# Kernel tuning notes

Measured on AMD Instinct MI355X. Metric: run time of the kernel, lower is better.

Reference implementation:

```python
import jax, jax.numpy as jnp
import numpy as np

N_NODES = 100000
N_EDGES = 1600000
F_IN, HIDDEN, N_CLASS = 256, 64, 2


def _gcn_conv(x, W, b, src, dst, norm, n):
    # PyG GCNConv: linear (no bias) -> normalized scatter-add -> bias
    h = x @ W                                  # [N, out]
    msg = h[src] * norm[:, None]               # gather + scale, [E+N, out]
    agg = jax.ops.segment_sum(msg, dst, num_segments=n)
    return agg + b


def setup_inputs() -> dict:
    key = jax.random.key(0)
    ks = jax.random.split(key, 8)
    x = jax.random.normal(ks[0], (N_NODES, F_IN), dtype=jnp.float32)
    edge_index = jax.random.randint(ks[1], (2, N_EDGES), 0, N_NODES, dtype=jnp.int32)
    W1 = jax.random.normal(ks[2], (F_IN, HIDDEN), dtype=jnp.float32) / np.sqrt(F_IN).astype(np.float32)
    b1 = jnp.zeros((HIDDEN,), dtype=jnp.float32)
    W2 = jax.random.normal(ks[3], (HIDDEN, HIDDEN), dtype=jnp.float32) / np.sqrt(HIDDEN).astype(np.float32)
    b2 = jnp.zeros((HIDDEN,), dtype=jnp.float32)
    W3 = jax.random.normal(ks[4], (HIDDEN, N_CLASS), dtype=jnp.float32) / np.sqrt(HIDDEN).astype(np.float32)
    b3 = jnp.zeros((N_CLASS,), dtype=jnp.float32)
    return {"x": x, "edge_index": edge_index, "W1": W1, "b1": b1, "W2": W2, "b2": b2, "W3": W3, "b3": b3}


def reference(x, edge_index, W1, b1, W2, b2, W3, b3):
    n = x.shape[0]
    # add self-loops (GCNConv default)
    loops = jnp.arange(n, dtype=edge_index.dtype)
    src = jnp.concatenate([edge_index[0], loops])
    dst = jnp.concatenate([edge_index[1], loops])
    # symmetric normalization D^-1/2 A_hat D^-1/2
    deg = jax.ops.segment_sum(jnp.ones_like(src, dtype=x.dtype), dst, num_segments=n)
    deg_inv_sqrt = jnp.where(deg > 0, jax.lax.rsqrt(jnp.maximum(deg, 1.0)), 0.0)
    norm = deg_inv_sqrt[src] * deg_inv_sqrt[dst]
    # layer 1 + relu (dropout is identity in eval mode)
    h = jax.nn.relu(_gcn_conv(x, W1, b1, src, dst, norm, n))
    # layer 2 + relu
    h = jax.nn.relu(_gcn_conv(h, W2, b2, src, dst, norm, n))
    # output layer + log_softmax
    h = _gcn_conv(h, W3, b3, src, dst, norm, n)
    return jax.nn.log_softmax(h, axis=1)
```

## Files before the change

kernel.cpp:

```cpp
#include <hip/hip_runtime.h>
#include <math.h>

#define F_IN 256
#define HID  64
#define BSH  8
#define BSPAN 256
#define CHUNK 4096
#define NBK_MAX 512

typedef __bf16   bf16x8 __attribute__((ext_vector_type(8)));
typedef float    floatx4 __attribute__((ext_vector_type(4)));
typedef _Float16 half8 __attribute__((ext_vector_type(8)));
typedef _Float16 half4v __attribute__((ext_vector_type(4)));

__global__ __launch_bounds__(256) void k_hist(const int* __restrict__ dst,
                                              int* __restrict__ cntT,
                                              int E, int NCH, int NBK) {
    __shared__ int hist[NBK_MAX];
    int t = threadIdx.x, c = blockIdx.x;
    hist[t] = 0; hist[t + 256] = 0;
    __syncthreads();
    int base = c * CHUNK;
#pragma unroll 4
    for (int j = 0; j < CHUNK / 256; j++) {
        int e = base + j * 256 + t;
        if (e < E) atomicAdd(&hist[dst[e] >> BSH], 1);
    }
    __syncthreads();
    for (int b = t; b < NBK; b += 256) cntT[b * NCH + c] = hist[b];
}

__global__ __launch_bounds__(256) void k_scanA(const int* __restrict__ cntT,
                                               int* __restrict__ off,
                                               int* __restrict__ partials, int S) {
    __shared__ int sh[256];
    int tid = threadIdx.x;
    int base = blockIdx.x * 1024 + tid * 4;
    int v[4];
    int s = 0;
#pragma unroll
    for (int j = 0; j < 4; j++) {
        int idx = base + j;
        v[j] = (idx < S) ? cntT[idx] : 0;
        s += v[j];
    }
    sh[tid] = s;
    __syncthreads();
    int mysum = s;
    for (int o = 1; o < 256; o <<= 1) {
        int tv = (tid >= o) ? sh[tid - o] : 0;
        __syncthreads();
        sh[tid] += tv;
        __syncthreads();
    }
    int pref = sh[tid] - mysum;
#pragma unroll
    for (int j = 0; j < 4; j++) {
        int idx = base + j;
        if (idx < S) off[idx] = pref;
        pref += v[j];
    }
    if (tid == 255) partials[blockIdx.x] = sh[255];
}

__global__ void k_scanB(int* __restrict__ partials, int* __restrict__ off,
                        int nblk, int S) {
    if (blockIdx.x == 0 && threadIdx.x == 0) {
        int run = 0;
        for (int b = 0; b < nblk; b++) { int t = partials[b]; partials[b] = run; run += t; }
        off[S] = run;
    }
}

__global__ void k_scanC(int* __restrict__ off, const int* __restrict__ partials, int S) {
    int i = blockIdx.x * blockDim.x + threadIdx.x;
    if (i < S) off[i] += partials[i >> 10];
}

__global__ __launch_bounds__(256) void k_sortwrite(const int* __restrict__ src,
                                                   const int* __restrict__ dst,
                                                   const int* __restrict__ off,
                                                   int* __restrict__ ebuf,
                                                   int E, int NCH, int NBK) {
    __shared__ int cur[NBK_MAX];
    int t = threadIdx.x, c = blockIdx.x;
    for (int b = t; b < NBK; b += 256) cur[b] = off[b * NCH + c];
    __syncthreads();
    int base = c * CHUNK;
#pragma unroll 4
    for (int j = 0; j < CHUNK / 256; j++) {
        int e = base + j * 256 + t;
        if (e < E) {
            int s = src[e];
            int d = dst[e];
            int pos = atomicAdd(&cur[d >> BSH], 1);
            ebuf[pos] = (s << BSH) | (d & (BSPAN - 1));
        }
    }
}

__global__ __launch_bounds__(256) void k_bucket_csr(const int* __restrict__ off,
                                                    const int* __restrict__ ebuf,
                                                    int* __restrict__ rp,
                                                    float* __restrict__ dinv,
                                                    int* __restrict__ esrc,
                                                    int N, int NCH, int NBK) {
    __shared__ int cnt[BSPAN];
    __shared__ int sh[BSPAN];
    int b = blockIdx.x, t = threadIdx.x;
    int base = off[b * NCH];
    int end  = off[(b + 1) * NCH];

    cnt[t] = 0;
    __syncthreads();
    for (int i = base + t; i < end; i += 256) atomicAdd(&cnt[ebuf[i] & (BSPAN - 1)], 1);
    __syncthreads();

    int c = cnt[t];
    sh[t] = c;
    __syncthreads();
    for (int o = 1; o < 256; o <<= 1) {
        int tv = (t >= o) ? sh[t - o] : 0;
        __syncthreads();
        sh[t] += tv;
        __syncthreads();
    }
    int excl = sh[t] - c;

    int node = (b << BSH) + t;
    if (node < N) {
        rp[node] = base + excl;
        dinv[node] = rsqrtf((float)(1 + c));
    }
    if (b == NBK - 1 && t == 0) rp[N] = end;
    __syncthreads();

    cnt[t] = base + excl;
    __syncthreads();
    for (int i = base + t; i < end; i += 256) {
        int v = ebuf[i];
        int p = atomicAdd(&cnt[v & (BSPAN - 1)], 1);
        esrc[p] = v >> BSH;
    }
}

__global__ __launch_bounds__(256) void k_prepw(const float* __restrict__ W1,
                                               __bf16* __restrict__ f1h, __bf16* __restrict__ f1l,
                                               const float* __restrict__ W2,
                                               __bf16* __restrict__ f2h, __bf16* __restrict__ f2l) {
    int t = threadIdx.x + blockIdx.x * blockDim.x;
    for (int idx = t; idx < 16384; idx += 2048) {
        int j = idx & 7, lane = (idx >> 3) & 63, ch2 = (idx >> 9) & 7, c = idx >> 12;
        int k = ch2 * 32 + (lane >> 4) * 8 + j, col = c * 16 + (lane & 15);
        float w = W1[k * 64 + col];
        __bf16 h = (__bf16)w;
        f1h[idx] = h; f1l[idx] = (__bf16)(w - (float)h);
    }
    for (int idx = t; idx < 4096; idx += 2048) {
        int j = idx & 7, lane = (idx >> 3) & 63, ch2 = (idx >> 9) & 1, c = idx >> 10;
        int k = ch2 * 32 + (lane >> 4) * 8 + j, col = c * 16 + (lane & 15);
        float w = W2[k * 64 + col];
        __bf16 h = (__bf16)w;
        f2h[idx] = h; f2l[idx] = (__bf16)(w - (float)h);
    }
}

__global__ __launch_bounds__(256) void k_gemm1(const float* __restrict__ A,
                                               const __bf16* __restrict__ BfH,
                                               const __bf16* __restrict__ BfL,
                                               const float* __restrict__ dinv,
                                               _Float16* __restrict__ C, int nrows) {
    constexpr int K = 256, KC = 64, NCHK = 4, NCH32 = 8;
    __shared__ float As[2][64 * KC];

    const int t = threadIdx.x;
    const int wave = t >> 6, lane = t & 63;
    const int m = lane & 15, q = lane >> 4;
    const int row0 = blockIdx.x * 64;

    const int s_sub = lane >> 4;
    const int s_seg = lane & 15;

    auto stage = [&](int ch, int buf) {
#pragma unroll
        for (int j = 0; j < 4; j++) {
            int lr = wave * 16 + j * 4 + s_sub;
            int gr = row0 + lr; if (gr > nrows - 1) gr = nrows - 1;
            int gs = (s_seg - lr) & 15;
            const float* g = A + (size_t)gr * K + ch * KC + gs * 4;
            float* l = &As[buf][(size_t)lr * KC + s_seg * 4];
            __builtin_amdgcn_global_load_lds(
                (const __attribute__((address_space(1))) void*)g,
                (__attribute__((address_space(3))) void*)l, 16, 0, 0);
        }
    };

    floatx4 acc[4] = {{0.f, 0.f, 0.f, 0.f}, {0.f, 0.f, 0.f, 0.f},
                      {0.f, 0.f, 0.f, 0.f}, {0.f, 0.f, 0.f, 0.f}};

    stage(0, 0);
    __syncthreads();

    for (int ch = 0; ch < NCHK; ch++) {
        if (ch + 1 < NCHK) stage(ch + 1, (ch + 1) & 1);

        const float* arow = &As[ch & 1][(size_t)(wave * 16 + m) * KC];
#pragma unroll
        for (int jj = 0; jj < 2; jj++) {
            int ch2 = ch * 2 + jj;
            int s0 = jj * 8 + q * 2;
            float4 v0 = *(const float4*)(arow + (((s0 + m) & 15) * 4));
            float4 v1 = *(const float4*)(arow + (((s0 + 1 + m) & 15) * 4));
            float af[8] = {v0.x, v0.y, v0.z, v0.w, v1.x, v1.y, v1.z, v1.w};
            bf16x8 ah, al;
#pragma unroll
            for (int j = 0; j < 8; j++) {
                __bf16 h = (__bf16)af[j];
                ah[j] = h;
                al[j] = (__bf16)(af[j] - (float)h);
            }
#pragma unroll
            for (int c = 0; c < 4; c++) {
                const bf16x8 bh = *(const bf16x8*)(BfH + ((size_t)(c * NCH32 + ch2) * 64 + lane) * 8);
                const bf16x8 bl = *(const bf16x8*)(BfL + ((size_t)(c * NCH32 + ch2) * 64 + lane) * 8);
                acc[c] = __builtin_amdgcn_mfma_f32_16x16x32_bf16(ah, bh, acc[c], 0, 0, 0);
                acc[c] = __builtin_amdgcn_mfma_f32_16x16x32_bf16(al, bh, acc[c], 0, 0, 0);
                acc[c] = __builtin_amdgcn_mfma_f32_16x16x32_bf16(ah, bl, acc[c], 0, 0, 0);
            }
        }
        __syncthreads();
    }

#pragma unroll
    for (int i = 0; i < 4; i++) {
        int r = row0 + wave * 16 + q * 4 + i;
        if (r < nrows) {
            float di = dinv[r];
#pragma unroll
            for (int c = 0; c < 4; c++)
                C[(size_t)r * 64 + c * 16 + m] = (_Float16)(acc[c][i] * di);
        }
    }
}

__global__ __launch_bounds__(256) void k_gemm2(const _Float16* __restrict__ A,
                                               const __bf16* __restrict__ BfH,
                                               const __bf16* __restrict__ BfL,
                                               const float* __restrict__ dinv,
                                               _Float16* __restrict__ C, int nrows) {
    __shared__ _Float16 As[64 * 64];
    const int t = threadIdx.x;
    const int wave = t >> 6, lane = t & 63;
    const int m = lane & 15, q = lane >> 4;
    const int row0 = blockIdx.x * 64;

#pragma unroll
    for (int j = 0; j < 2; j++) {
        int lr = j * 32 + wave * 8 + (lane >> 3);
        int p  = lane & 7;
        int gr = row0 + lr; if (gr > nrows - 1) gr = nrows - 1;
        int gs = (p - lr) & 7;
        const _Float16* g = A + (size_t)gr * 64 + gs * 8;
        _Float16* l = &As[(size_t)lr * 64 + p * 8];
        __builtin_amdgcn_global_load_lds(
            (const __attribute__((address_space(1))) void*)g,
            (__attribute__((address_space(3))) void*)l, 16, 0, 0);
    }
    __syncthreads();

    floatx4 acc[4] = {{0.f, 0.f, 0.f, 0.f}, {0.f, 0.f, 0.f, 0.f},
                      {0.f, 0.f, 0.f, 0.f}, {0.f, 0.f, 0.f, 0.f}};

    const _Float16* arow = &As[(size_t)(wave * 16 + m) * 64];
#pragma unroll
    for (int jj = 0; jj < 2; jj++) {
        int s0 = jj * 4 + q;
        half8 v = *(const half8*)(arow + (((s0 + m) & 7) * 8));
        bf16x8 ah, al;
#pragma unroll
        for (int j = 0; j < 8; j++) {
            float f = (float)v[j];
            __bf16 h = (__bf16)f;
            ah[j] = h;
            al[j] = (__bf16)(f - (float)h);
        }
#pragma unroll
        for (int c = 0; c < 4; c++) {
            const bf16x8 bh = *(const bf16x8*)(BfH + ((size_t)(c * 2 + jj) * 64 + lane) * 8);
            const bf16x8 bl = *(const bf16x8*)(BfL + ((size_t)(c * 2 + jj) * 64 + lane) * 8);
            acc[c] = __builtin_amdgcn_mfma_f32_16x16x32_bf16(ah, bh, acc[c], 0, 0, 0);
            acc[c] = __builtin_amdgcn_mfma_f32_16x16x32_bf16(al, bh, acc[c], 0, 0, 0);
            acc[c] = __builtin_amdgcn_mfma_f32_16x16x32_bf16(ah, bl, acc[c], 0, 0, 0);
        }
    }

#pragma unroll
    for (int i = 0; i < 4; i++) {
        int r = row0 + wave * 16 + q * 4 + i;
        if (r < nrows) {
            float di = dinv[r];
#pragma unroll
            for (int c = 0; c < 4; c++)
                C[(size_t)r * 64 + c * 16 + m] = (_Float16)(acc[c][i] * di);
        }
    }
}

template <int MODE>
__global__ __launch_bounds__(256) void k_agg64(const _Float16* __restrict__ hs,
                                               const float* __restrict__ dinv,
                                               const int* __restrict__ rp,
                                               const int* __restrict__ esrc,
                                               const float* __restrict__ bias,
                                               const float* __restrict__ W3,
                                               void* __restrict__ out, int n) {
    int lane = threadIdx.x & 63;
    int qe = lane >> 4;
    int fg = lane & 15;
    int nid = blockIdx.x * 4 + (threadIdx.x >> 6);
    if (nid >= n) return;
    nid = __builtin_amdgcn_readfirstlane(nid);

    float dii = dinv[nid];
    int e0 = rp[nid];
    int e1 = rp[nid + 1];
    int last = e1 - 1;

    float a0 = 0.f, a1 = 0.f, a2 = 0.f, a3 = 0.f;
    if (qe == 0) {
        half4v sv = *(const half4v*)(hs + (size_t)nid * 64 + fg * 4);
        a0 = (float)sv[0]; a1 = (float)sv[1]; a2 = (float)sv[2]; a3 = (float)sv[3];
    }

    for (int e = e0; e <= last; e += 16) {
#pragma unroll
        for (int u = 0; u < 4; u++) {
            int slot = e + u * 4 + qe;
            int idx = esrc[min(slot, last)];
            half4v v = *(const half4v*)(hs + (size_t)idx * 64 + fg * 4);
            if (slot <= last) {
                a0 += (float)v[0]; a1 += (float)v[1];
                a2 += (float)v[2]; a3 += (float)v[3];
            }
        }
    }

#pragma unroll
    for (int o = 16; o <= 32; o <<= 1) {
        a0 += __shfl_xor(a0, o, 64);
        a1 += __shfl_xor(a1, o, 64);
        a2 += __shfl_xor(a2, o, 64);
        a3 += __shfl_xor(a3, o, 64);
    }

    float4 b4 = ((const float4*)bias)[fg];
    a0 = fmaxf(a0 * dii + b4.x, 0.f);
    a1 = fmaxf(a1 * dii + b4.y, 0.f);
    a2 = fmaxf(a2 * dii + b4.z, 0.f);
    a3 = fmaxf(a3 * dii + b4.w, 0.f);

    if (MODE == 0) {
        if (qe == 0) {
            half4v o4;
            o4[0] = (_Float16)a0; o4[1] = (_Float16)a1;
            o4[2] = (_Float16)a2; o4[3] = (_Float16)a3;
            *(half4v*)((_Float16*)out + (size_t)nid * 64 + fg * 4) = o4;
        }
    } else {
        const float2* w3 = (const float2*)W3;
        float2 w0 = w3[fg * 4 + 0], w1 = w3[fg * 4 + 1];
        float2 w2 = w3[fg * 4 + 2], w3v = w3[fg * 4 + 3];
        float p0 = a0 * w0.x + a1 * w1.x + a2 * w2.x + a3 * w3v.x;
        float p1 = a0 * w0.y + a1 * w1.y + a2 * w2.y + a3 * w3v.y;
#pragma unroll
        for (int o = 1; o <= 8; o <<= 1) {
            p0 += __shfl_xor(p0, o, 64);
            p1 += __shfl_xor(p1, o, 64);
        }
        if (lane == 0) ((float2*)out)[nid] = make_float2(p0 * dii, p1 * dii);
    }
}

__global__ __launch_bounds__(256) void k_final(const float2* __restrict__ h3s,
                                               const float* __restrict__ dinv,
                                               const int* __restrict__ rp,
                                               const int* __restrict__ esrc,
                                               const float* __restrict__ b3,
                                               float* __restrict__ out, int n) {
    int i = blockIdx.x * blockDim.x + threadIdx.x;
    if (i >= n) return;
    float dii = dinv[i];
    float2 h = h3s[i];
    float ax = h.x, ay = h.y;
    float bx = 0.f, by = 0.f, cx = 0.f, cy = 0.f, dx = 0.f, dy = 0.f;
    int e0 = rp[i], e1 = rp[i + 1];
    for (int e = e0; e < e1; e += 4) {
        int last = e1 - 1;
        int s0 = esrc[e];
        int s1 = esrc[min(e + 1, last)];
        int s2 = esrc[min(e + 2, last)];
        int s3 = esrc[min(e + 3, last)];
        float2 v0 = h3s[s0];
        float2 v1 = h3s[s1];
        float2 v2 = h3s[s2];
        float2 v3 = h3s[s3];
        ax += v0.x; ay += v0.y;
        bx += (e + 1 <= last) ? v1.x : 0.f; by += (e + 1 <= last) ? v1.y : 0.f;
        cx += (e + 2 <= last) ? v2.x : 0.f; cy += (e + 2 <= last) ? v2.y : 0.f;
        dx += (e + 3 <= last) ? v3.x : 0.f; dy += (e + 3 <= last) ? v3.y : 0.f;
    }
    float l0 = ((ax + bx) + (cx + dx)) * dii + b3[0];
    float l1 = ((ay + by) + (cy + dy)) * dii + b3[1];
    float mx = fmaxf(l0, l1);
    float lse = mx + log1pf(__expf(-fabsf(l0 - l1)));
    ((float2*)out)[i] = make_float2(l0 - lse, l1 - lse);
}

extern "C" void kernel_launch(void* const* d_in, const int* in_sizes, int n_in,
                              void* d_out, int out_size, void* d_ws, size_t ws_size,
                              hipStream_t stream) {
    const float* x   = (const float*)d_in[0];
    const int*   ei  = (const int*)d_in[1];
    const float* W1  = (const float*)d_in[2];
    const float* b1  = (const float*)d_in[3];
    const float* W2  = (const float*)d_in[4];
    const float* b2  = (const float*)d_in[5];
    const float* W3  = (const float*)d_in[6];
    const float* b3  = (const float*)d_in[7];
    float* out = (float*)d_out;

    const int N = in_sizes[0] / F_IN;
    const int E = in_sizes[1] / 2;
    const int* src = ei;
    const int* dst = ei + E;

    const int NBK = (N + BSPAN - 1) / BSPAN;
    const int NCH = (E + CHUNK - 1) / CHUNK;
    const int S   = NBK * NCH;

    char* p = (char*)d_ws;
    auto alloc = [&](size_t bytes) -> void* {
        void* r = (void*)p;
        p += (bytes + 255) & ~(size_t)255;
        return r;
    };
    int*      cntT     = (int*)alloc((size_t)S * 4);
    int*      off      = (int*)alloc((size_t)(S + 1) * 4);
    int*      partials = (int*)alloc(4096);
    int*      ebuf     = (int*)alloc((size_t)E * 4);
    int*      esrc     = (int*)alloc((size_t)E * 4);
    int*      rp       = (int*)alloc((size_t)(N + 1) * 4);
    float*    dinv     = (float*)alloc((size_t)N * 4);
    _Float16* bufA     = (_Float16*)alloc((size_t)N * HID * 2);
    _Float16* bufB     = (_Float16*)alloc((size_t)N * HID * 2);
    float*    h3       = (float*)alloc((size_t)N * 2 * 4);
    __bf16*   f1h      = (__bf16*)alloc(16384 * 2);
    __bf16*   f1l      = (__bf16*)alloc(16384 * 2);
    __bf16*   f2h      = (__bf16*)alloc(4096 * 2);
    __bf16*   f2l      = (__bf16*)alloc(4096 * 2);

    const int T = 256;
    int scanBlocks = (S + 1023) / 1024;

    k_prepw<<<8, T, 0, stream>>>(W1, f1h, f1l, W2, f2h, f2l);

    k_hist<<<NCH, T, 0, stream>>>(dst, cntT, E, NCH, NBK);
    k_scanA<<<scanBlocks, T, 0, stream>>>(cntT, off, partials, S);
    k_scanB<<<1, 64, 0, stream>>>(partials, off, scanBlocks, S);
    k_scanC<<<(S + T - 1) / T, T, 0, stream>>>(off, partials, S);
    k_sortwrite<<<NCH, T, 0, stream>>>(src, dst, off, ebuf, E, NCH, NBK);
    k_bucket_csr<<<NBK, T, 0, stream>>>(off, ebuf, rp, dinv, esrc, N, NCH, NBK);

    int gemmBlocks = (N + 63) / 64;
    k_gemm1<<<gemmBlocks, T, 0, stream>>>(x, f1h, f1l, dinv, bufA, N);
    k_agg64<0><<<(N + 3) / 4, T, 0, stream>>>(bufA, dinv, rp, esrc, b1, nullptr, bufB, N);

    k_gemm2<<<gemmBlocks, T, 0, stream>>>(bufB, f2h, f2l, dinv, bufA, N);
    k_agg64<1><<<(N + 3) / 4, T, 0, stream>>>(bufA, dinv, rp, esrc, b2, W3, h3, N);

    k_final<<<(N + T - 1) / T, T, 0, stream>>>((const float2*)h3, dinv, rp, esrc, b3, out, N);
}
```

Measured before the change: 407.2 us.

## Switch aggregation to edge-balanced blocks with packed dst row and LDS atomics

Aggregation now gives each 64-node block an equal slice of its CSR edge range instead of one wavefront per node. Each sub-group walks its edges and keeps a run-length partial sum per destination row, which it flushes with LDS atomics. The edge source index is packed with the local destination row in the low 6 bits. Intermediate features from both GEMMs are stored in fp32 instead of fp16, doubling gather traffic but removing conversions. The intent is to remove load imbalance from uneven degrees; the cost is LDS atomic contention and larger feature reads.

```diff
diff --git a/kernel.cpp b/kernel.cpp
--- a/kernel.cpp
+++ b/kernel.cpp
@@ -132,7 +132,10 @@
         rp[node] = base + excl;
         dinv[node] = rsqrtf((float)(1 + c));
     }
-    if (b == NBK - 1 && t == 0) rp[N] = end;
+    if (b == NBK - 1) {
+        if (t == 0) rp[N] = end;
+        if (t < 16) esrc[end + t] = 0;
+    }
     __syncthreads();
 
     cnt[t] = base + excl;
@@ -140,7 +143,7 @@
     for (int i = base + t; i < end; i += 256) {
         int v = ebuf[i];
         int p = atomicAdd(&cnt[v & (BSPAN - 1)], 1);
-        esrc[p] = v >> BSH;
+        esrc[p] = ((v >> BSH) << 6) | (v & 63);
     }
 }
 
@@ -169,7 +172,7 @@
                                                const __bf16* __restrict__ BfH,
                                                const __bf16* __restrict__ BfL,
                                                const float* __restrict__ dinv,
-                                               _Float16* __restrict__ C, int nrows) {
+                                               float* __restrict__ C, int nrows) {
     constexpr int K = 256, KC = 64, NCHK = 4, NCH32 = 8;
     __shared__ float As[2][64 * KC];
 
@@ -238,7 +241,7 @@
             float di = dinv[r];
 #pragma unroll
             for (int c = 0; c < 4; c++)
-                C[(size_t)r * 64 + c * 16 + m] = (_Float16)(acc[c][i] * di);
+                C[(size_t)r * 64 + c * 16 + m] = acc[c][i] * di;
         }
     }
 }
@@ -247,7 +250,7 @@
                                                const __bf16* __restrict__ BfH,
                                                const __bf16* __restrict__ BfL,
                                                const float* __restrict__ dinv,
-                                               _Float16* __restrict__ C, int nrows) {
+                                               float* __restrict__ C, int nrows) {
     __shared__ _Float16 As[64 * 64];
     const int t = threadIdx.x;
     const int wave = t >> 6, lane = t & 63;
@@ -301,83 +304,110 @@
             float di = dinv[r];
 #pragma unroll
             for (int c = 0; c < 4; c++)
-                C[(size_t)r * 64 + c * 16 + m] = (_Float16)(acc[c][i] * di);
+                C[(size_t)r * 64 + c * 16 + m] = acc[c][i] * di;
         }
     }
 }
 
 template <int MODE>
-__global__ __launch_bounds__(256) void k_agg64(const _Float16* __restrict__ hs,
-                                               const float* __restrict__ dinv,
-                                               const int* __restrict__ rp,
-                                               const int* __restrict__ esrc,
-                                               const float* __restrict__ bias,
-                                               const float* __restrict__ W3,
-                                               void* __restrict__ out, int n) {
-    int lane = threadIdx.x & 63;
-    int qe = lane >> 4;
-    int fg = lane & 15;
-    int nid = blockIdx.x * 4 + (threadIdx.x >> 6);
-    if (nid >= n) return;
-    nid = __builtin_amdgcn_readfirstlane(nid);
-
-    float dii = dinv[nid];
-    int e0 = rp[nid];
-    int e1 = rp[nid + 1];
-    int last = e1 - 1;
-
-    float a0 = 0.f, a1 = 0.f, a2 = 0.f, a3 = 0.f;
-    if (qe == 0) {
-        half4v sv = *(const half4v*)(hs + (size_t)nid * 64 + fg * 4);
-        a0 = (float)sv[0]; a1 = (float)sv[1]; a2 = (float)sv[2]; a3 = (float)sv[3];
-    }
-
-    for (int e = e0; e <= last; e += 16) {
+__global__ __launch_bounds__(256) void k_aggE(const float* __restrict__ hs,
+                                              const float* __restrict__ dinv,
+                                              const int* __restrict__ rp,
+                                              const int* __restrict__ esrc,
+                                              const float* __restrict__ bias,
+                                              const float* __restrict__ W3,
+                                              void* __restrict__ out, int n) {
+    constexpr int NPB = 64;
+    constexpr int LDW = 68;
+    __shared__ float acc[NPB * LDW];
+
+    const int t = threadIdx.x;
+    const int wv = t >> 6, lane = t & 63;
+    const int qe = lane >> 4, fg = lane & 15;
+    const int nb = blockIdx.x * NPB;
+    const int ne = min(nb + NPB, n);
+
+    for (int i = t; i < NPB * LDW; i += 256) acc[i] = 0.f;
+
+    const int eb0 = rp[nb];
+    const int eb1 = rp[ne];
+    __syncthreads();
+
+    const int L  = eb1 - eb0;
+    const int wl = (L + 3) >> 2;
+    const int wa = eb0 + wv * wl;
+    const int wb = min(wa + wl, eb1);
+    const int ql = (wl + 3) >> 2;
+    const int qa = wa + qe * ql;
+    const int qb = min(qa + ql, wb);
+
+    int cur = -1;
+    floatx4 r = {0.f, 0.f, 0.f, 0.f};
+    for (int e = qa; e < qb; e += 4) {
 #pragma unroll
         for (int u = 0; u < 4; u++) {
-            int slot = e + u * 4 + qe;
-            int idx = esrc[min(slot, last)];
-            half4v v = *(const half4v*)(hs + (size_t)idx * 64 + fg * 4);
-            if (slot <= last) {
-                a0 += (float)v[0]; a1 += (float)v[1];
-                a2 += (float)v[2]; a3 += (float)v[3];
+            int ev = esrc[e + u];
+            int row = ev & 63;
+            floatx4 v = *(const floatx4*)(hs + (size_t)(ev >> 6) * 64 + fg * 4);
+            if (e + u < qb) {
+                if (row != cur) {
+                    if (cur >= 0) {
+                        float* a = &acc[cur * LDW + fg * 4];
+                        atomicAdd(a + 0, r[0]); atomicAdd(a + 1, r[1]);
+                        atomicAdd(a + 2, r[2]); atomicAdd(a + 3, r[3]);
+                    }
+                    cur = row; r = v;
+                } else {
+                    r[0] += v[0]; r[1] += v[1]; r[2] += v[2]; r[3] += v[3];
+                }
             }
         }
     }
-
-#pragma unroll
-    for (int o = 16; o <= 32; o <<= 1) {
-        a0 += __shfl_xor(a0, o, 64);
-        a1 += __shfl_xor(a1, o, 64);
-        a2 += __shfl_xor(a2, o, 64);
-        a3 += __shfl_xor(a3, o, 64);
-    }
-
-    float4 b4 = ((const float4*)bias)[fg];
-    a0 = fmaxf(a0 * dii + b4.x, 0.f);
-    a1 = fmaxf(a1 * dii + b4.y, 0.f);
-    a2 = fmaxf(a2 * dii + b4.z, 0.f);
-    a3 = fmaxf(a3 * dii + b4.w, 0.f);
+    if (cur >= 0) {
+        float* a = &acc[cur * LDW + fg * 4];
+        atomicAdd(a + 0, r[0]); atomicAdd(a + 1, r[1]);
+        atomicAdd(a + 2, r[2]); atomicAdd(a + 3, r[3]);
+    }
+    __syncthreads();
 
     if (MODE == 0) {
-        if (qe == 0) {
-            half4v o4;
-            o4[0] = (_Float16)a0; o4[1] = (_Float16)a1;
-            o4[2] = (_Float16)a2; o4[3] = (_Float16)a3;
-            *(half4v*)((_Float16*)out + (size_t)nid * 64 + fg * 4) = o4;
+#pragma unroll
+        for (int it = 0; it < 4; it++) {
+            int nl = it * 16 + (t >> 4);
+            int node = nb + nl;
+            if (node < n) {
+                int f = (t & 15) * 4;
+                float dii = dinv[node];
+                floatx4 av = *(const floatx4*)&acc[nl * LDW + f];
+                floatx4 sv = *(const floatx4*)(hs + (size_t)node * 64 + f);
+                float4 b4 = ((const float4*)bias)[t & 15];
+                float v0 = fmaxf((av[0] + sv[0]) * dii + b4.x, 0.f);
+                float v1 = fmaxf((av[1] + sv[1]) * dii + b4.y, 0.f);
+                float v2 = fmaxf((av[2] + sv[2]) * dii + b4.z, 0.f);
+                float v3 = fmaxf((av[3] + sv[3]) * dii + b4.w, 0.f);
+                half4v o4;
+                o4[0] = (_Float16)v0; o4[1] = (_Float16)v1;
+                o4[2] = (_Float16)v2; o4[3] = (_Float16)v3;
+                *(half4v*)((_Float16*)out + (size_t)node * 64 + f) = o4;
+            }
         }
     } else {
-        const float2* w3 = (const float2*)W3;
-        float2 w0 = w3[fg * 4 + 0], w1 = w3[fg * 4 + 1];
-        float2 w2 = w3[fg * 4 + 2], w3v = w3[fg * 4 + 3];
-        float p0 = a0 * w0.x + a1 * w1.x + a2 * w2.x + a3 * w3v.x;
-        float p1 = a0 * w0.y + a1 * w1.y + a2 * w2.y + a3 * w3v.y;
-#pragma unroll
-        for (int o = 1; o <= 8; o <<= 1) {
-            p0 += __shfl_xor(p0, o, 64);
-            p1 += __shfl_xor(p1, o, 64);
-        }
-        if (lane == 0) ((float2*)out)[nid] = make_float2(p0 * dii, p1 * dii);
+        for (int it = 0; it < 16; it++) {
+            int nl = it * 4 + wv;
+            int node = nb + nl;
+            if (node >= n) break;
+            float dii = dinv[node];
+            float a = acc[nl * LDW + lane] + hs[(size_t)node * 64 + lane];
+            a = fmaxf(a * dii + bias[lane], 0.f);
+            float2 w = ((const float2*)W3)[lane];
+            float p0 = a * w.x, p1 = a * w.y;
+#pragma unroll
+            for (int o = 1; o <= 32; o <<= 1) {
+                p0 += __shfl_xor(p0, o, 64);
+                p1 += __shfl_xor(p1, o, 64);
+            }
+            if (lane == 0) ((float2*)out)[node] = make_float2(p0 * dii, p1 * dii);
+        }
     }
 }
 
@@ -396,10 +426,10 @@
     int e0 = rp[i], e1 = rp[i + 1];
     for (int e = e0; e < e1; e += 4) {
         int last = e1 - 1;
-        int s0 = esrc[e];
-        int s1 = esrc[min(e + 1, last)];
-        int s2 = esrc[min(e + 2, last)];
-        int s3 = esrc[min(e + 3, last)];
+        int s0 = esrc[e] >> 6;
+        int s1 = esrc[min(e + 1, last)] >> 6;
+        int s2 = esrc[min(e + 2, last)] >> 6;
+        int s3 = esrc[min(e + 3, last)] >> 6;
         float2 v0 = h3s[s0];
         float2 v1 = h3s[s1];
         float2 v2 = h3s[s2];
@@ -448,10 +478,10 @@
     int*      off      = (int*)alloc((size_t)(S + 1) * 4);
     int*      partials = (int*)alloc(4096);
     int*      ebuf     = (int*)alloc((size_t)E * 4);
-    int*      esrc     = (int*)alloc((size_t)E * 4);
+    int*      esrc     = (int*)alloc((size_t)(E + 64) * 4);
     int*      rp       = (int*)alloc((size_t)(N + 1) * 4);
     float*    dinv     = (float*)alloc((size_t)N * 4);
-    _Float16* bufA     = (_Float16*)alloc((size_t)N * HID * 2);
+    float*    h32      = (float*)alloc((size_t)N * HID * 4);
     _Float16* bufB     = (_Float16*)alloc((size_t)N * HID * 2);
     float*    h3       = (float*)alloc((size_t)N * 2 * 4);
     __bf16*   f1h      = (__bf16*)alloc(16384 * 2);
@@ -472,11 +502,12 @@
     k_bucket_csr<<<NBK, T, 0, stream>>>(off, ebuf, rp, dinv, esrc, N, NCH, NBK);
 
     int gemmBlocks = (N + 63) / 64;
-    k_gemm1<<<gemmBlocks, T, 0, stream>>>(x, f1h, f1l, dinv, bufA, N);
-    k_agg64<0><<<(N + 3) / 4, T, 0, stream>>>(bufA, dinv, rp, esrc, b1, nullptr, bufB, N);
-
-    k_gemm2<<<gemmBlocks, T, 0, stream>>>(bufB, f2h, f2l, dinv, bufA, N);
-    k_agg64<1><<<(N + 3) / 4, T, 0, stream>>>(bufA, dinv, rp, esrc, b2, W3, h3, N);
+    int aggBlocks  = (N + 63) / 64;
+    k_gemm1<<<gemmBlocks, T, 0, stream>>>(x, f1h, f1l, dinv, h32, N);
+    k_aggE<0><<<aggBlocks, T, 0, stream>>>(h32, dinv, rp, esrc, b1, nullptr, bufB, N);
+
+    k_gemm2<<<gemmBlocks, T, 0, stream>>>(bufB, f2h, f2l, dinv, h32, N);
+    k_aggE<1><<<aggBlocks, T, 0, stream>>>(h32, dinv, rp, esrc, b2, W3, h3, N);
 
     k_final<<<(N + T - 1) / T, T, 0, stream>>>((const float2*)h3, dinv, rp, esrc, b3, out, N);
 }
```

Measured after the change: 430.3 us. +5.7%, slower.

## Fuse layer-1 aggregation with layer-2 GEMM and merge weight prep into histogram

Applied to the files above, without the earlier changes.

Layer-1 neighbor aggregation now runs inside a 64-row block that keeps the ReLU'd fp32 rows in shared memory and immediately applies the split-bf16 MFMA GEMM with W2. This removes the fp16 round trip of the intermediate through global memory and one kernel launch. The weight-prep kernel is folded into the histogram kernel's first 8 blocks, saving another launch. The trade-off is that each wave now aggregates 16 rows serially within a block, which lowers parallelism for the gather stage. The esrc buffer is also padded with zeros at its tail.

```diff
diff --git a/kernel.cpp b/kernel.cpp
--- a/kernel.cpp
+++ b/kernel.cpp
@@ -10,12 +10,15 @@
 
 typedef __bf16   bf16x8 __attribute__((ext_vector_type(8)));
 typedef float    floatx4 __attribute__((ext_vector_type(4)));
-typedef _Float16 half8 __attribute__((ext_vector_type(8)));
 typedef _Float16 half4v __attribute__((ext_vector_type(4)));
 
-__global__ __launch_bounds__(256) void k_hist(const int* __restrict__ dst,
-                                              int* __restrict__ cntT,
-                                              int E, int NCH, int NBK) {
+__global__ __launch_bounds__(256) void k_pre(const int* __restrict__ dst,
+                                             int* __restrict__ cntT,
+                                             int E, int NCH, int NBK,
+                                             const float* __restrict__ W1,
+                                             __bf16* __restrict__ f1h, __bf16* __restrict__ f1l,
+                                             const float* __restrict__ W2,
+                                             __bf16* __restrict__ f2h, __bf16* __restrict__ f2l) {
     __shared__ int hist[NBK_MAX];
     int t = threadIdx.x, c = blockIdx.x;
     hist[t] = 0; hist[t + 256] = 0;
@@ -28,6 +31,24 @@
     }
     __syncthreads();
     for (int b = t; b < NBK; b += 256) cntT[b * NCH + c] = hist[b];
+
+    if (c < 8) {
+        int g = c * 256 + t;
+        for (int idx = g; idx < 16384; idx += 2048) {
+            int j = idx & 7, lane = (idx >> 3) & 63, ch2 = (idx >> 9) & 7, cc = idx >> 12;
+            int k = ch2 * 32 + (lane >> 4) * 8 + j, col = cc * 16 + (lane & 15);
+            float w = W1[k * 64 + col];
+            __bf16 h = (__bf16)w;
+            f1h[idx] = h; f1l[idx] = (__bf16)(w - (float)h);
+        }
+        for (int idx = g; idx < 4096; idx += 2048) {
+            int j = idx & 7, lane = (idx >> 3) & 63, ch2 = (idx >> 9) & 1, cc = idx >> 10;
+            int k = ch2 * 32 + (lane >> 4) * 8 + j, col = cc * 16 + (lane & 15);
+            float w = W2[k * 64 + col];
+            __bf16 h = (__bf16)w;
+            f2h[idx] = h; f2l[idx] = (__bf16)(w - (float)h);
+        }
+    }
 }
 
 __global__ __launch_bounds__(256) void k_scanA(const int* __restrict__ cntT,
@@ -132,7 +153,10 @@
         rp[node] = base + excl;
         dinv[node] = rsqrtf((float)(1 + c));
     }
-    if (b == NBK - 1 && t == 0) rp[N] = end;
+    if (b == NBK - 1) {
+        if (t == 0) rp[N] = end;
+        if (t < 16) esrc[end + t] = 0;
+    }
     __syncthreads();
 
     cnt[t] = base + excl;
@@ -141,27 +165,6 @@
         int v = ebuf[i];
         int p = atomicAdd(&cnt[v & (BSPAN - 1)], 1);
         esrc[p] = v >> BSH;
-    }
-}
-
-__global__ __launch_bounds__(256) void k_prepw(const float* __restrict__ W1,
-                                               __bf16* __restrict__ f1h, __bf16* __restrict__ f1l,
-                                               const float* __restrict__ W2,
-                                               __bf16* __restrict__ f2h, __bf16* __restrict__ f2l) {
-    int t = threadIdx.x + blockIdx.x * blockDim.x;
-    for (int idx = t; idx < 16384; idx += 2048) {
-        int j = idx & 7, lane = (idx >> 3) & 63, ch2 = (idx >> 9) & 7, c = idx >> 12;
-        int k = ch2 * 32 + (lane >> 4) * 8 + j, col = c * 16 + (lane & 15);
-        float w = W1[k * 64 + col];
-        __bf16 h = (__bf16)w;
-        f1h[idx] = h; f1l[idx] = (__bf16)(w - (float)h);
-    }
-    for (int idx = t; idx < 4096; idx += 2048) {
-        int j = idx & 7, lane = (idx >> 3) & 63, ch2 = (idx >> 9) & 1, c = idx >> 10;
-        int k = ch2 * 32 + (lane >> 4) * 8 + j, col = c * 16 + (lane & 15);
-        float w = W2[k * 64 + col];
-        __bf16 h = (__bf16)w;
-        f2h[idx] = h; f2l[idx] = (__bf16)(w - (float)h);
     }
 }
 
@@ -243,46 +246,86 @@
     }
 }
 
-__global__ __launch_bounds__(256) void k_gemm2(const _Float16* __restrict__ A,
-                                               const __bf16* __restrict__ BfH,
-                                               const __bf16* __restrict__ BfL,
-                                               const float* __restrict__ dinv,
-                                               _Float16* __restrict__ C, int nrows) {
-    __shared__ _Float16 As[64 * 64];
+__global__ __launch_bounds__(256) void k_aggG(const _Float16* __restrict__ hs,
+                                              const float* __restrict__ dinv,
+                                              const int* __restrict__ rp,
+                                              const int* __restrict__ esrc,
+                                              const float* __restrict__ bias,
+                                              const __bf16* __restrict__ BfH,
+                                              const __bf16* __restrict__ BfL,
+                                              _Float16* __restrict__ C, int n) {
+    constexpr int LDW = 68;
+    __shared__ float As[64 * LDW];
+
     const int t = threadIdx.x;
     const int wave = t >> 6, lane = t & 63;
+    const int qe = lane >> 4, fg = lane & 15;
+    const int row0 = blockIdx.x * 64;
+
+    for (int i = 0; i < 16; i++) {
+        int row = wave * 16 + i;
+        int nid = row0 + row;
+        if (nid < n) {
+            float dii = dinv[nid];
+            int e0 = rp[nid];
+            int e1 = rp[nid + 1];
+            int last = e1 - 1;
+
+            float a0 = 0.f, a1 = 0.f, a2 = 0.f, a3 = 0.f;
+            if (qe == 0) {
+                half4v sv = *(const half4v*)(hs + (size_t)nid * 64 + fg * 4);
+                a0 = (float)sv[0]; a1 = (float)sv[1]; a2 = (float)sv[2]; a3 = (float)sv[3];
+            }
+            for (int e = e0; e <= last; e += 16) {
+#pragma unroll
+                for (int u = 0; u < 4; u++) {
+                    int slot = e + u * 4 + qe;
+                    int idx = esrc[min(slot, last)];
+                    half4v v = *(const half4v*)(hs + (size_t)idx * 64 + fg * 4);
+                    if (slot <= last) {
+                        a0 += (float)v[0]; a1 += (float)v[1];
+                        a2 += (float)v[2]; a3 += (float)v[3];
+                    }
+                }
+            }
+#pragma unroll
+            for (int o = 16; o <= 32; o <<= 1) {
+                a0 += __shfl_xor(a0, o, 64);
+                a1 += __shfl_xor(a1, o, 64);
+                a2 += __shfl_xor(a2, o, 64);
+                a3 += __shfl_xor(a3, o, 64);
+            }
+            if (qe == 0) {
+                float4 b4 = ((const float4*)bias)[fg];
+                float* r = &As[row * LDW + fg * 4];
+                r[0] = fmaxf(a0 * dii + b4.x, 0.f);
+                r[1] = fmaxf(a1 * dii + b4.y, 0.f);
+                r[2] = fmaxf(a2 * dii + b4.z, 0.f);
+                r[3] = fmaxf(a3 * dii + b4.w, 0.f);
+            }
+        } else if (qe == 0) {
+            float* r = &As[row * LDW + fg * 4];
+            r[0] = 0.f; r[1] = 0.f; r[2] = 0.f; r[3] = 0.f;
+        }
+    }
+    __syncthreads();
+
     const int m = lane & 15, q = lane >> 4;
-    const int row0 = blockIdx.x * 64;
-
-#pragma unroll
-    for (int j = 0; j < 2; j++) {
-        int lr = j * 32 + wave * 8 + (lane >> 3);
-        int p  = lane & 7;
-        int gr = row0 + lr; if (gr > nrows - 1) gr = nrows - 1;
-        int gs = (p - lr) & 7;
-        const _Float16* g = A + (size_t)gr * 64 + gs * 8;
-        _Float16* l = &As[(size_t)lr * 64 + p * 8];
-        __builtin_amdgcn_global_load_lds(
-            (const __attribute__((address_space(1))) void*)g,
-            (__attribute__((address_space(3))) void*)l, 16, 0, 0);
-    }
-    __syncthreads();
-
     floatx4 acc[4] = {{0.f, 0.f, 0.f, 0.f}, {0.f, 0.f, 0.f, 0.f},
                       {0.f, 0.f, 0.f, 0.f}, {0.f, 0.f, 0.f, 0.f}};
 
-    const _Float16* arow = &As[(size_t)(wave * 16 + m) * 64];
+    const float* arow = &As[(size_t)(wave * 16 + m) * LDW];
 #pragma unroll
     for (int jj = 0; jj < 2; jj++) {
-        int s0 = jj * 4 + q;
-        half8 v = *(const half8*)(arow + (((s0 + m) & 7) * 8));
+        float4 v0 = *(const float4*)(arow + jj * 32 + q * 8);
+        float4 v1 = *(const float4*)(arow + jj * 32 + q * 8 + 4);
+        float af[8] = {v0.x, v0.y, v0.z, v0.w, v1.x, v1.y, v1.z, v1.w};
         bf16x8 ah, al;
 #pragma unroll
         for (int j = 0; j < 8; j++) {
-            float f = (float)v[j];
-            __bf16 h = (__bf16)f;
+            __bf16 h = (__bf16)af[j];
             ah[j] = h;
-            al[j] = (__bf16)(f - (float)h);
+            al[j] = (__bf16)(af[j] - (float)h);
         }
 #pragma unroll
         for (int c = 0; c < 4; c++) {
@@ -297,7 +340,7 @@
 #pragma unroll
     for (int i = 0; i < 4; i++) {
         int r = row0 + wave * 16 + q * 4 + i;
-        if (r < nrows) {
+        if (r < n) {
             float di = dinv[r];
 #pragma unroll
             for (int c = 0; c < 4; c++)
@@ -306,14 +349,13 @@
     }
 }
 
-template <int MODE>
-__global__ __launch_bounds__(256) void k_agg64(const _Float16* __restrict__ hs,
-                                               const float* __restrict__ dinv,
-                                               const int* __restrict__ rp,
-                                               const int* __restrict__ esrc,
-                                               const float* __restrict__ bias,
-                                               const float* __restrict__ W3,
-                                               void* __restrict__ out, int n) {
+__global__ __launch_bounds__(256) void k_agg3(const _Float16* __restrict__ hs,
+                                              const float* __restrict__ dinv,
+                                              const int* __restrict__ rp,
+                                              const int* __restrict__ esrc,
+                                              const float* __restrict__ bias,
+                                              const float* __restrict__ W3,
+                                              float2* __restrict__ out, int n) {
     int lane = threadIdx.x & 63;
     int qe = lane >> 4;
     int fg = lane & 15;
@@ -359,26 +401,17 @@
     a2 = fmaxf(a2 * dii + b4.z, 0.f);
     a3 = fmaxf(a3 * dii + b4.w, 0.f);
 
-    if (MODE == 0) {
-        if (qe == 0) {
-            half4v o4;
-            o4[0] = (_Float16)a0; o4[1] = (_Float16)a1;
-            o4[2] = (_Float16)a2; o4[3] = (_Float16)a3;
-            *(half4v*)((_Float16*)out + (size_t)nid * 64 + fg * 4) = o4;
-        }
-    } else {
-        const float2* w3 = (const float2*)W3;
-        float2 w0 = w3[fg * 4 + 0], w1 = w3[fg * 4 + 1];
-        float2 w2 = w3[fg * 4 + 2], w3v = w3[fg * 4 + 3];
-        float p0 = a0 * w0.x + a1 * w1.x + a2 * w2.x + a3 * w3v.x;
-        float p1 = a0 * w0.y + a1 * w1.y + a2 * w2.y + a3 * w3v.y;
-#pragma unroll
-        for (int o = 1; o <= 8; o <<= 1) {
-            p0 += __shfl_xor(p0, o, 64);
-            p1 += __shfl_xor(p1, o, 64);
-        }
-        if (lane == 0) ((float2*)out)[nid] = make_float2(p0 * dii, p1 * dii);
-    }
+    const float2* w3 = (const float2*)W3;
+    float2 w0 = w3[fg * 4 + 0], w1 = w3[fg * 4 + 1];
+    float2 w2 = w3[fg * 4 + 2], w3v = w3[fg * 4 + 3];
+    float p0 = a0 * w0.x + a1 * w1.x + a2 * w2.x + a3 * w3v.x;
+    float p1 = a0 * w0.y + a1 * w1.y + a2 * w2.y + a3 * w3v.y;
+#pragma unroll
+    for (int o = 1; o <= 8; o <<= 1) {
+        p0 += __shfl_xor(p0, o, 64);
+        p1 += __shfl_xor(p1, o, 64);
+    }
+    if (lane == 0) out[nid] = make_float2(p0 * dii, p1 * dii);
 }
 
 __global__ __launch_bounds__(256) void k_final(const float2* __restrict__ h3s,
@@ -448,7 +481,7 @@
     int*      off      = (int*)alloc((size_t)(S + 1) * 4);
     int*      partials = (int*)alloc(4096);
     int*      ebuf     = (int*)alloc((size_t)E * 4);
-    int*      esrc     = (int*)alloc((size_t)E * 4);
+    int*      esrc     = (int*)alloc((size_t)(E + 64) * 4);
     int*      rp       = (int*)alloc((size_t)(N + 1) * 4);
     float*    dinv     = (float*)alloc((size_t)N * 4);
     _Float16* bufA     = (_Float16*)alloc((size_t)N * HID * 2);
@@ -462,9 +495,7 @@
     const int T = 256;
     int scanBlocks = (S + 1023) / 1024;
 
-    k_prepw<<<8, T, 0, stream>>>(W1, f1h, f1l, W2, f2h, f2l);
-
-    k_hist<<<NCH, T, 0, stream>>>(dst, cntT, E, NCH, NBK);
+    k_pre<<<NCH, T, 0, stream>>>(dst, cntT, E, NCH, NBK, W1, f1h, f1l, W2, f2h, f2l);
     k_scanA<<<scanBlocks, T, 0, stream>>>(cntT, off, partials, S);
     k_scanB<<<1, 64, 0, stream>>>(partials, off, scanBlocks, S);
     k_scanC<<<(S + T - 1) / T, T, 0, stream>>>(off, partials, S);
@@ -473,10 +504,10 @@
 
     int gemmBlocks = (N + 63) / 64;
     k_gemm1<<<gemmBlocks, T, 0, stream>>>(x, f1h, f1l, dinv, bufA, N);
-    k_agg64<0><<<(N + 3) / 4, T, 0, stream>>>(bufA, dinv, rp, esrc, b1, nullptr, bufB, N);
-
-    k_gemm2<<<gemmBlocks, T, 0, stream>>>(bufB, f2h, f2l, dinv, bufA, N);
-    k_agg64<1><<<(N + 3) / 4, T, 0, stream>>>(bufA, dinv, rp, esrc, b2, W3, h3, N);
+
+    k_aggG<<<gemmBlocks, T, 0, stream>>>(bufA, dinv, rp, esrc, b1, f2h, f2l, bufB, N);
+
+    k_agg3<<<(N + 3) / 4, T, 0, stream>>>(bufB, dinv, rp, esrc, b2, W3, (float2*)h3, N);
 
     k_final<<<(N + T - 1) / T, T, 0, stream>>>((const float2*)h3, dinv, rp, esrc, b3, out, N);
 }
```

Result: slower. 451.8 us (+11.0%).
